# Optimization experiments

Hardware: AMD Instinct MI355X
Metric: run time of the kernel (lower is better)

The kernel has to match this reference:

```python
import jax, jax.numpy as jnp
import numpy as np

WEIGHT_BITS = 4           # weight_bit_width for both convs
SCALE_MIN = 2e-16         # scaling_min_val from CommonIntWeightPerTensorQuant


def fake_quant_per_channel(w, bits):
    """Brevitas-style per-output-channel symmetric narrow-range int fake quant.
    scale = max|w| over each output channel / (2^(bits-1) - 1), STE round."""
    qmax = float(2 ** (bits - 1) - 1)
    absmax = jnp.max(jnp.abs(w.reshape(w.shape[0], -1)), axis=1)
    scale = jnp.maximum(absmax / qmax, SCALE_MIN)
    scale = scale.reshape((-1,) + (1,) * (w.ndim - 1))
    q = jnp.clip(jnp.round(w / scale), -qmax, qmax) * scale
    # straight-through estimator (matches brevitas round_ste)
    return w + jax.lax.stop_gradient(q - w)


def setup_inputs() -> dict:
    key = jax.random.key(0)
    k1, k2, k3, k4 = jax.random.split(key, 4)
    x = jax.random.normal(k1, (32, 384, 56, 56), dtype=jnp.float32)
    # depthwise weight: (out=C, in/groups=1, kH, kW)
    dw_w = jax.random.normal(k2, (384, 1, 3, 3), dtype=jnp.float32) * 0.1
    # pointwise weight: (out, in, 1, 1); pw conv has default bias=True
    pw_w = jax.random.normal(k3, (384, 384, 1, 1), dtype=jnp.float32) * 0.05
    pw_b = jax.random.normal(k4, (384,), dtype=jnp.float32) * 0.01
    return {"x": x, "dw_w": dw_w, "pw_w": pw_w, "pw_b": pw_b}


def reference(x, dw_w, pw_w, pw_b):
    C = dw_w.shape[0]
    dw_q = fake_quant_per_channel(dw_w, WEIGHT_BITS)
    pw_q = fake_quant_per_channel(pw_w, WEIGHT_BITS)
    # depthwise 3x3, stride 1, pad 1
    y = jax.lax.conv_general_dilated(
        x, dw_q, window_strides=(1, 1), padding=((1, 1), (1, 1)),
        dimension_numbers=("NCHW", "OIHW", "NCHW"), feature_group_count=C)
    # pointwise 1x1 + bias
    z = jax.lax.conv_general_dilated(
        y, pw_q, window_strides=(1, 1), padding="VALID",
        dimension_numbers=("NCHW", "OIHW", "NCHW"))
    return z + pw_b[None, :, None, None]
```

## Files before the change

### kernel.cpp

```cpp
#include <hip/hip_runtime.h>
#include <hip/hip_bf16.h>

#define CCH 384
#define HW2 3136
#define HH 56
#define WW 56
#define QMAX 7.0f
#define SCALE_MIN 2e-16f
#define PB 49
#define YSLAB 512
#define YPB 24576
#define ROWP 60
#define CHW 964

typedef _Float16 half8 __attribute__((ext_vector_type(8)));
typedef float f32x4 __attribute__((ext_vector_type(4)));

#define GLOAD_LDS16(g, l) __builtin_amdgcn_global_load_lds( \
    (const __attribute__((address_space(1))) void*)(g), \
    (__attribute__((address_space(3))) void*)(l), 16, 0, 0)


__global__ void quant_dw(const float* __restrict__ dw, float* __restrict__ dwq) {
    int c = blockIdx.x * blockDim.x + threadIdx.x;
    if (c >= CCH) return;
    float w[9];
    float amax = 0.f;
    #pragma unroll
    for (int j = 0; j < 9; ++j) {
        w[j] = dw[c * 9 + j];
        amax = fmaxf(amax, fabsf(w[j]));
    }
    float scale = fmaxf(amax / QMAX, SCALE_MIN);
    #pragma unroll
    for (int j = 0; j < 9; ++j) {
        float q = rintf(w[j] / scale);
        q = fminf(fmaxf(q, -QMAX), QMAX);
        dwq[c * 9 + j] = q * scale;
    }
}

__global__ void quant_pw(const float* __restrict__ pw, _Float16* __restrict__ wpk) {
    int co = blockIdx.x;
    int lane = threadIdx.x;
    float w[6];
    float amax = 0.f;
    #pragma unroll
    for (int j = 0; j < 6; ++j) {
        w[j] = pw[co * CCH + lane + j * 64];
        amax = fmaxf(amax, fabsf(w[j]));
    }
    #pragma unroll
    for (int off = 32; off >= 1; off >>= 1)
        amax = fmaxf(amax, __shfl_xor(amax, off));
    float scale = fmaxf(amax / QMAX, SCALE_MIN);
    #pragma unroll
    for (int j = 0; j < 6; ++j) {
        int ci = lane + j * 64;
        float q = rintf(w[j] / scale);
        q = fminf(fmaxf(q, -QMAX), QMAX);
        float v = q * scale;
        int kk  = ci >> 5;
        int cis = ci & 31;
        int l   = (co & 15) | ((cis >> 3) << 4);
        int idx = (kk * 24 + (co >> 4)) * 512 + l * 8 + (cis & 7);
        wpk[idx] = (_Float16)v;
    }
}


__global__ __launch_bounds__(128) void dw_kernel(
    const float* __restrict__ x, const float* __restrict__ dwq,
    _Float16* __restrict__ ypk)
{
    __shared__ __align__(16) float xs[8 * CHW];

    int bid = blockIdx.x;
    int wg = (bid & 7) * 768 + (bid >> 3);
    int rg = wg & 3;
    int t2 = wg >> 2;
    int c8 = t2 % 48, n = t2 / 48;
    const int h0 = rg * 14;
    const int tid = threadIdx.x;

    const float* xpl = x + ((size_t)n * CCH + (size_t)c8 * 8) * HW2;

    {
        int s = tid >> 3, ch = tid & 7;
        *(f32x4*)&xs[ch * CHW + 4 + s * ROWP + 56] = (f32x4){0.f, 0.f, 0.f, 0.f};
        if (tid < 32) xs[(tid >> 2) * CHW + (tid & 3)] = 0.f;
    }

    {
        const int ch = tid >> 4, idx16 = tid & 15;
        const float* src = xpl + (size_t)ch * HW2;
        #pragma unroll
        for (int j = 0; j < 14; ++j) {
            const int g = j * 16 + idx16;
            const int s = g / 14, q = g - s * 14;
            const int srow = h0 - 1 + s;
            const int crow = srow < 0 ? 0 : (srow > 55 ? 55 : srow);
            f32x4 v = *(const f32x4*)(src + crow * WW + q * 4);
            if (srow != crow) v = (f32x4){0.f, 0.f, 0.f, 0.f};
            *(f32x4*)&xs[ch * CHW + 4 + s * ROWP + q * 4] = v;
        }
    }
    __syncthreads();

    if (tid >= 98) return;

    const int row  = tid / 7;
    const int wseg = tid - row * 7;
    const int w0   = wseg * 8;
    const int qlo  = (w0 - 1) >> 2;

    half8 pk[8];
    #pragma unroll
    for (int ch = 0; ch < 8; ++ch) {
        const float* wq = dwq + (size_t)(c8 * 8 + ch) * 9;
        float wv[9];
        #pragma unroll
        for (int k = 0; k < 9; ++k) wv[k] = wq[k];

        float a[8] = {0.f,0.f,0.f,0.f,0.f,0.f,0.f,0.f};
        #pragma unroll
        for (int dr = 0; dr < 3; ++dr) {
            const int base = ch * CHW + 4 + (row + dr) * ROWP + qlo * 4;
            f32x4 q0 = *(const f32x4*)&xs[base];
            f32x4 q1 = *(const f32x4*)&xs[base + 4];
            f32x4 q2 = *(const f32x4*)&xs[base + 8];
            f32x4 q3 = *(const f32x4*)&xs[base + 12];
            float win[16] = {q0.x,q0.y,q0.z,q0.w, q1.x,q1.y,q1.z,q1.w,
                             q2.x,q2.y,q2.z,q2.w, q3.x,q3.y,q3.z,q3.w};
            #pragma unroll
            for (int j0 = 0; j0 < 8; ++j0) {
                float s0 = a[j0];
                s0 = fmaf(win[3 + j0], wv[dr * 3 + 0], s0);
                s0 = fmaf(win[4 + j0], wv[dr * 3 + 1], s0);
                s0 = fmaf(win[5 + j0], wv[dr * 3 + 2], s0);
                a[j0] = s0;
            }
        }
        #pragma unroll
        for (int j0 = 0; j0 < 8; ++j0) pk[j0][ch] = (_Float16)a[j0];
    }

    const int posb = (h0 + row) * WW + w0;
    _Float16* yn = ypk + (size_t)n * PB * YPB + (size_t)c8 * YSLAB;
    #pragma unroll
    for (int j0 = 0; j0 < 8; ++j0) {
        const int pos = posb + j0;
        *(half8*)(yn + (size_t)(pos >> 6) * YPB + (pos & 63) * 8) = pk[j0];
    }
}


__global__ __launch_bounds__(256) void pw_kernel(
    const _Float16* __restrict__ ypk, const _Float16* __restrict__ wpk,
    const float* __restrict__ bias, float* __restrict__ out)
{
    __shared__ __align__(16) _Float16 ysh[YPB];

    int bid = blockIdx.x;
    int wg = (bid & 7) * 196 + (bid >> 3);
    int n = wg / PB, pb = wg % PB;

    const int t = threadIdx.x;
    const int lane = t & 63;
    const int g = __builtin_amdgcn_readfirstlane(t >> 6);

    const _Float16* yg = ypk + (size_t)(n * PB + pb) * YPB;
    #pragma unroll
    for (int j = 0; j < 12; ++j) {
        GLOAD_LDS16(yg + (j * 256 + t) * 8,
                    ysh + (size_t)(j * 256 + (t & 192)) * 8);
    }
    __syncthreads();

    const int lco = lane & 15;
    const int lkg = lane >> 4;
    const int cbf = g * 6;

    f32x4 acc[6][4];
    #pragma unroll
    for (int mc = 0; mc < 6; ++mc)
        #pragma unroll
        for (int np = 0; np < 4; ++np)
            acc[mc][np] = (f32x4){0.f, 0.f, 0.f, 0.f};

    for (int kk = 0; kk < 12; ++kk) {
        half8 wf[6];
        #pragma unroll
        for (int mc = 0; mc < 6; ++mc)
            wf[mc] = *(const half8*)(wpk + (size_t)(kk * 24 + cbf + mc) * 512 + lane * 8);
        half8 yf[4];
        #pragma unroll
        for (int np = 0; np < 4; ++np)
            yf[np] = *(const half8*)(ysh + kk * 2048 + lkg * 512 + (np * 16 + lco) * 8);
        #pragma unroll
        for (int mc = 0; mc < 6; ++mc)
            #pragma unroll
            for (int np = 0; np < 4; ++np)
                acc[mc][np] = __builtin_amdgcn_mfma_f32_16x16x32_f16(
                    wf[mc], yf[np], acc[mc][np], 0, 0, 0);
    }

    float* ob = out + (size_t)n * CCH * HW2 + (size_t)pb * 64;
    #pragma unroll
    for (int mc = 0; mc < 6; ++mc) {
        #pragma unroll
        for (int r = 0; r < 4; ++r) {
            const int co = g * 96 + mc * 16 + lkg * 4 + r;
            const float bv = bias[co];
            #pragma unroll
            for (int np = 0; np < 4; ++np)
                ob[(size_t)co * HW2 + np * 16 + lco] = acc[mc][np][r] + bv;
        }
    }
}


extern "C" void kernel_launch(void* const* d_in, const int* in_sizes, int n_in,
                              void* d_out, int out_size, void* d_ws, size_t ws_size,
                              hipStream_t stream) {
    const float* x  = (const float*)d_in[0];
    const float* dw = (const float*)d_in[1];
    const float* pw = (const float*)d_in[2];
    const float* pb = (const float*)d_in[3];
    float* out = (float*)d_out;

    float*    dwq = (float*)d_ws;
    _Float16* wpk = (_Float16*)(dwq + CCH * 9);
    _Float16* ypk = wpk + (size_t)CCH * CCH;

    quant_dw<<<2, 256, 0, stream>>>(dw, dwq);
    quant_pw<<<CCH, 64, 0, stream>>>(pw, wpk);

    dw_kernel<<<6144, 128, 0, stream>>>(x, dwq, ypk);
    pw_kernel<<<1568, 256, 0, stream>>>(ypk, wpk, pb, out);
}
```

Baseline: 126.0 us.

## Loop dw row groups per block with register prefetch; pw reads y directly, vectorized stores

```diff
diff --git a/kernel.cpp b/kernel.cpp
--- a/kernel.cpp
+++ b/kernel.cpp
@@ -16,10 +16,6 @@
 typedef _Float16 half8 __attribute__((ext_vector_type(8)));
 typedef float f32x4 __attribute__((ext_vector_type(4)));
 
-#define GLOAD_LDS16(g, l) __builtin_amdgcn_global_load_lds( \
-    (const __attribute__((address_space(1))) void*)(g), \
-    (__attribute__((address_space(3))) void*)(l), 16, 0, 0)
-
 
 __global__ void quant_dw(const float* __restrict__ dw, float* __restrict__ dwq) {
     int c = blockIdx.x * blockDim.x + threadIdx.x;
@@ -76,11 +72,8 @@
     __shared__ __align__(16) float xs[8 * CHW];
 
     int bid = blockIdx.x;
-    int wg = (bid & 7) * 768 + (bid >> 3);
-    int rg = wg & 3;
-    int t2 = wg >> 2;
-    int c8 = t2 % 48, n = t2 / 48;
-    const int h0 = rg * 14;
+    int wg = (bid & 7) * 192 + (bid >> 3);
+    int c8 = wg % 48, n = wg / 48;
     const int tid = threadIdx.x;
 
     const float* xpl = x + ((size_t)n * CCH + (size_t)c8 * 8) * HW2;
@@ -91,66 +84,94 @@
         if (tid < 32) xs[(tid >> 2) * CHW + (tid & 3)] = 0.f;
     }
 
-    {
-        const int ch = tid >> 4, idx16 = tid & 15;
-        const float* src = xpl + (size_t)ch * HW2;
-        #pragma unroll
-        for (int j = 0; j < 14; ++j) {
-            const int g = j * 16 + idx16;
-            const int s = g / 14, q = g - s * 14;
-            const int srow = h0 - 1 + s;
-            const int crow = srow < 0 ? 0 : (srow > 55 ? 55 : srow);
-            f32x4 v = *(const f32x4*)(src + crow * WW + q * 4);
-            if (srow != crow) v = (f32x4){0.f, 0.f, 0.f, 0.f};
-            *(f32x4*)&xs[ch * CHW + 4 + s * ROWP + q * 4] = v;
-        }
-    }
-    __syncthreads();
-
-    if (tid >= 98) return;
+    const int sch = tid >> 4, idx16 = tid & 15;
+    const float* src = xpl + (size_t)sch * HW2;
 
     const int row  = tid / 7;
     const int wseg = tid - row * 7;
     const int w0   = wseg * 8;
     const int qlo  = (w0 - 1) >> 2;
 
-    half8 pk[8];
-    #pragma unroll
-    for (int ch = 0; ch < 8; ++ch) {
-        const float* wq = dwq + (size_t)(c8 * 8 + ch) * 9;
-        float wv[9];
-        #pragma unroll
-        for (int k = 0; k < 9; ++k) wv[k] = wq[k];
-
-        float a[8] = {0.f,0.f,0.f,0.f,0.f,0.f,0.f,0.f};
-        #pragma unroll
-        for (int dr = 0; dr < 3; ++dr) {
-            const int base = ch * CHW + 4 + (row + dr) * ROWP + qlo * 4;
-            f32x4 q0 = *(const f32x4*)&xs[base];
-            f32x4 q1 = *(const f32x4*)&xs[base + 4];
-            f32x4 q2 = *(const f32x4*)&xs[base + 8];
-            f32x4 q3 = *(const f32x4*)&xs[base + 12];
-            float win[16] = {q0.x,q0.y,q0.z,q0.w, q1.x,q1.y,q1.z,q1.w,
-                             q2.x,q2.y,q2.z,q2.w, q3.x,q3.y,q3.z,q3.w};
+    _Float16* yn = ypk + (size_t)n * PB * YPB + (size_t)c8 * YSLAB;
+
+    f32x4 v[14];
+    #pragma unroll
+    for (int j = 0; j < 14; ++j) {
+        const int gq = j * 16 + idx16;
+        const int s = gq / 14, q = gq - s * 14;
+        const int srow = -1 + s;
+        const int crow = srow < 0 ? 0 : srow;
+        f32x4 t = *(const f32x4*)(src + crow * WW + q * 4);
+        if (srow != crow) t = (f32x4){0.f, 0.f, 0.f, 0.f};
+        v[j] = t;
+    }
+
+    #pragma unroll
+    for (int rg = 0; rg < 4; ++rg) {
+        const int h0 = rg * 14;
+
+        #pragma unroll
+        for (int j = 0; j < 14; ++j) {
+            const int gq = j * 16 + idx16;
+            const int s = gq / 14, q = gq - s * 14;
+            *(f32x4*)&xs[sch * CHW + 4 + s * ROWP + q * 4] = v[j];
+        }
+        __syncthreads();
+
+        if (rg < 3) {
+            const int h0n = h0 + 14;
+            #pragma unroll
+            for (int j = 0; j < 14; ++j) {
+                const int gq = j * 16 + idx16;
+                const int s = gq / 14, q = gq - s * 14;
+                const int srow = h0n - 1 + s;
+                const int crow = srow > 55 ? 55 : srow;
+                f32x4 t = *(const f32x4*)(src + crow * WW + q * 4);
+                if (srow != crow) t = (f32x4){0.f, 0.f, 0.f, 0.f};
+                v[j] = t;
+            }
+        }
+
+        if (tid < 98) {
+            half8 pk[8];
+            #pragma unroll
+            for (int ch = 0; ch < 8; ++ch) {
+                const float* wq = dwq + (size_t)(c8 * 8 + ch) * 9;
+                float wv[9];
+                #pragma unroll
+                for (int k = 0; k < 9; ++k) wv[k] = wq[k];
+
+                float a[8] = {0.f,0.f,0.f,0.f,0.f,0.f,0.f,0.f};
+                #pragma unroll
+                for (int dr = 0; dr < 3; ++dr) {
+                    const int base = ch * CHW + 4 + (row + dr) * ROWP + qlo * 4;
+                    f32x4 q0 = *(const f32x4*)&xs[base];
+                    f32x4 q1 = *(const f32x4*)&xs[base + 4];
+                    f32x4 q2 = *(const f32x4*)&xs[base + 8];
+                    f32x4 q3 = *(const f32x4*)&xs[base + 12];
+                    float win[16] = {q0.x,q0.y,q0.z,q0.w, q1.x,q1.y,q1.z,q1.w,
+                                     q2.x,q2.y,q2.z,q2.w, q3.x,q3.y,q3.z,q3.w};
+                    #pragma unroll
+                    for (int j0 = 0; j0 < 8; ++j0) {
+                        float s0 = a[j0];
+                        s0 = fmaf(win[3 + j0], wv[dr * 3 + 0], s0);
+                        s0 = fmaf(win[4 + j0], wv[dr * 3 + 1], s0);
+                        s0 = fmaf(win[5 + j0], wv[dr * 3 + 2], s0);
+                        a[j0] = s0;
+                    }
+                }
+                #pragma unroll
+                for (int j0 = 0; j0 < 8; ++j0) pk[j0][ch] = (_Float16)a[j0];
+            }
+
+            const int posb = (h0 + row) * WW + w0;
             #pragma unroll
             for (int j0 = 0; j0 < 8; ++j0) {
-                float s0 = a[j0];
-                s0 = fmaf(win[3 + j0], wv[dr * 3 + 0], s0);
-                s0 = fmaf(win[4 + j0], wv[dr * 3 + 1], s0);
-                s0 = fmaf(win[5 + j0], wv[dr * 3 + 2], s0);
-                a[j0] = s0;
+                const int pos = posb + j0;
+                *(half8*)(yn + (size_t)(pos >> 6) * YPB + (pos & 63) * 8) = pk[j0];
             }
         }
-        #pragma unroll
-        for (int j0 = 0; j0 < 8; ++j0) pk[j0][ch] = (_Float16)a[j0];
-    }
-
-    const int posb = (h0 + row) * WW + w0;
-    _Float16* yn = ypk + (size_t)n * PB * YPB + (size_t)c8 * YSLAB;
-    #pragma unroll
-    for (int j0 = 0; j0 < 8; ++j0) {
-        const int pos = posb + j0;
-        *(half8*)(yn + (size_t)(pos >> 6) * YPB + (pos & 63) * 8) = pk[j0];
+        __syncthreads();
     }
 }
 
@@ -159,8 +180,6 @@
     const _Float16* __restrict__ ypk, const _Float16* __restrict__ wpk,
     const float* __restrict__ bias, float* __restrict__ out)
 {
-    __shared__ __align__(16) _Float16 ysh[YPB];
-
     int bid = blockIdx.x;
     int wg = (bid & 7) * 196 + (bid >> 3);
     int n = wg / PB, pb = wg % PB;
@@ -170,12 +189,6 @@
     const int g = __builtin_amdgcn_readfirstlane(t >> 6);
 
     const _Float16* yg = ypk + (size_t)(n * PB + pb) * YPB;
-    #pragma unroll
-    for (int j = 0; j < 12; ++j) {
-        GLOAD_LDS16(yg + (j * 256 + t) * 8,
-                    ysh + (size_t)(j * 256 + (t & 192)) * 8);
-    }
-    __syncthreads();
 
     const int lco = lane & 15;
     const int lkg = lane >> 4;
@@ -196,25 +209,26 @@
         half8 yf[4];
         #pragma unroll
         for (int np = 0; np < 4; ++np)
-            yf[np] = *(const half8*)(ysh + kk * 2048 + lkg * 512 + (np * 16 + lco) * 8);
+            yf[np] = *(const half8*)(yg + kk * 2048 + lkg * 512 + (np * 16 + lco) * 8);
         #pragma unroll
         for (int mc = 0; mc < 6; ++mc)
             #pragma unroll
             for (int np = 0; np < 4; ++np)
                 acc[mc][np] = __builtin_amdgcn_mfma_f32_16x16x32_f16(
-                    wf[mc], yf[np], acc[mc][np], 0, 0, 0);
-    }
-
-    float* ob = out + (size_t)n * CCH * HW2 + (size_t)pb * 64;
+                    yf[np], wf[mc], acc[mc][np], 0, 0, 0);
+    }
+
     #pragma unroll
     for (int mc = 0; mc < 6; ++mc) {
-        #pragma unroll
-        for (int r = 0; r < 4; ++r) {
-            const int co = g * 96 + mc * 16 + lkg * 4 + r;
-            const float bv = bias[co];
-            #pragma unroll
-            for (int np = 0; np < 4; ++np)
-                ob[(size_t)co * HW2 + np * 16 + lco] = acc[mc][np][r] + bv;
+        const int co = g * 96 + mc * 16 + lco;
+        const float bv = bias[co];
+        float* orow = out + (size_t)n * CCH * HW2 + (size_t)co * HW2
+                          + (size_t)pb * 64 + lkg * 4;
+        #pragma unroll
+        for (int np = 0; np < 4; ++np) {
+            f32x4 v = acc[mc][np];
+            v.x += bv; v.y += bv; v.z += bv; v.w += bv;
+            *(f32x4*)(orow + np * 16) = v;
         }
     }
 }
@@ -236,6 +250,6 @@
     quant_dw<<<2, 256, 0, stream>>>(dw, dwq);
     quant_pw<<<CCH, 64, 0, stream>>>(pw, wpk);
 
-    dw_kernel<<<6144, 128, 0, stream>>>(x, dwq, ypk);
+    dw_kernel<<<1536, 128, 0, stream>>>(x, dwq, ypk);
     pw_kernel<<<1568, 256, 0, stream>>>(ypk, wpk, pb, out);
 }
```

Result: slower. 147.4 us (+17.0%).
